# Kernel tuning notes

Hardware: AMD Instinct MI355X
Metric: run time of the kernel (lower is better)

Reference implementation:

```python
import jax, jax.numpy as jnp
import numpy as np

B, L, D_EMB, D_K, D_V, N_HEAD = 32, 512, 768, 512, 1024, 8
LN_EPS = 1e-6
MASK_FILL = 1e-9  # non-standard fill value from the original module


def setup_inputs() -> dict:
    key = jax.random.key(0)
    ks = jax.random.split(key, 13)
    s = 0.02
    return {
        "q": jax.random.normal(ks[0], (B, L, D_EMB), jnp.float32),
        "k": jax.random.normal(ks[1], (B, L, D_EMB), jnp.float32),
        "v": jax.random.normal(ks[2], (B, L, D_EMB), jnp.float32),
        "Wq": jax.random.normal(ks[3], (D_EMB, D_K), jnp.float32) * s,
        "Wk": jax.random.normal(ks[4], (D_EMB, D_K), jnp.float32) * s,
        "Wv": jax.random.normal(ks[5], (D_EMB, D_V), jnp.float32) * s,
        "Wconv": jax.random.normal(ks[6], (D_K, D_K), jnp.float32) * s,  # Conv1d k=1 (out_ch, in_ch)
        "bconv": jax.random.normal(ks[7], (D_K,), jnp.float32) * s,
        "Wfc": jax.random.normal(ks[8], (D_V, D_EMB), jnp.float32) * s,
        "gamma": jnp.ones((D_EMB,), jnp.float32),
        "beta": jnp.zeros((D_EMB,), jnp.float32),
        "mask1": jax.random.randint(ks[9], (B, L), 0, 2).astype(jnp.bool_),
        "mask2": jax.random.randint(ks[10], (B, L), 0, 2).astype(jnp.bool_),
    }


def reference(q, k, v, Wq, Wk, Wv, Wconv, bconv, Wfc, gamma, beta, mask1, mask2):
    Bq, Lq, _ = q.shape
    Lk = k.shape[1]
    dh_k = D_K // N_HEAD
    dh_v = D_V // N_HEAD
    residual = q

    # Q/K projections followed by the (buggy-but-faithful) Conv1d(k=1) that
    # treats the sequence axis as channels: out[b,o,l] = sum_c W[o,c]*x[b,c,l] + bias[o]
    q1 = q @ Wq                                   # (B, Lq, D_K)
    k1 = k @ Wk                                   # (B, Lk, D_K)
    q1 = jnp.einsum('oc,bcl->bol', Wconv, q1) + bconv[None, :, None]
    k1 = jnp.einsum('oc,bcl->bol', Wconv, k1) + bconv[None, :, None]
    v1 = v @ Wv                                   # (B, Lk, D_V)

    qh = q1.reshape(Bq, Lq, N_HEAD, dh_k).transpose(0, 2, 1, 3)  # (B,H,Lq,dk/H)
    kh = k1.reshape(Bq, Lk, N_HEAD, dh_k).transpose(0, 2, 1, 3)
    vh = v1.reshape(Bq, Lk, N_HEAD, dh_v).transpose(0, 2, 1, 3)

    temp = jnp.sqrt(jnp.asarray(D_K, qh.dtype))
    attn = jnp.einsum('bhqd,bhkd->bhqk', qh / temp, kh)          # (B,H,Lq,Lk)
    attn = jnp.where(mask1[:, None, :, None], MASK_FILL, attn)
    attn = jnp.where(mask2[:, None, None, :], MASK_FILL, attn)
    attn = jax.nn.softmax(attn, axis=-1)
    # dropout is identity in eval / deterministic reference

    out = jnp.einsum('bhqk,bhkd->bhqd', attn, vh)                # (B,H,Lq,dv/H)
    out = out.transpose(0, 2, 1, 3).reshape(Bq, Lq, D_V)
    out = out @ Wfc + residual                                   # (B,Lq,D_EMB)

    mu = out.mean(-1, keepdims=True)
    var = out.var(-1, keepdims=True)
    out = (out - mu) / jnp.sqrt(var + LN_EPS) * gamma + beta
    out = jnp.where(jnp.isnan(out), jnp.zeros((), out.dtype), out)
    return out, attn
```

## Files before the change

kernel.cpp:

```cpp
#include <hip/hip_runtime.h>

typedef short v8s __attribute__((ext_vector_type(8)));
typedef short v4s __attribute__((ext_vector_type(4)));
typedef float v4f __attribute__((ext_vector_type(4)));

#define BN 128
#define BK 64

__device__ __forceinline__ float b2f(unsigned short u) {
    union { unsigned int i; float f; } x; x.i = ((unsigned int)u) << 16; return x.f;
}
__device__ __forceinline__ unsigned short f2b(float f) {
    union { float f; unsigned int i; } x; x.f = f;
    unsigned int r = x.i + 0x7fffu + ((x.i >> 16) & 1u);
    return (unsigned short)(r >> 16);
}

__device__ __forceinline__ void gload16(const void* g, void* l) {
    __builtin_amdgcn_global_load_lds(
        (const __attribute__((address_space(1))) void*)g,
        (__attribute__((address_space(3))) void*)l, 16, 0, 0);
}

template<int EPI>
__device__ __forceinline__ void gemm_body(
    const unsigned short* __restrict__ A, int lda, long aOff,
    const unsigned short* __restrict__ BT, int ldb, long bOff,
    void* __restrict__ C, int ldc, long cOff, long cSBt,
    int K, const float* __restrict__ bias,
    const float* __restrict__ resid, int ldr,
    int bm, int bn)
{
    __shared__ unsigned short SM[49152];

    const int tid = threadIdx.x;
    const int wave = tid >> 6, lane = tid & 63;
    const int wm = (wave >> 1) * 64, wn = (wave & 1) * 64;
    const int quad = lane >> 4, l16 = lane & 15;
    const int sx = l16 & 7;

    const unsigned short* aP[4]; const unsigned short* bP[2];
    int aL[4], bL[2];
#pragma unroll
    for (int p = 0; p < 4; p++) {
        int idx = p * 512 + tid;
        int row = idx >> 3, c = idx & 7, cc = c ^ (row & 7);
        aP[p] = A + aOff + (long)(bm + row) * lda + cc * 8;
        aL[p] = idx * 8;
    }
#pragma unroll
    for (int p = 0; p < 2; p++) {
        int idx = p * 512 + tid;
        int row = idx >> 3, c = idx & 7, cc = c ^ (row & 7);
        bP[p] = BT + bOff + (long)(bn + row) * ldb + cc * 8;
        bL[p] = 16384 + idx * 8;
    }

    auto stage = [&](int t, int b) {
        const int k0 = t * BK;
        unsigned short* base = &SM[b * 24576];
#pragma unroll
        for (int p = 0; p < 4; p++) gload16(aP[p] + k0, base + aL[p]);
#pragma unroll
        for (int p = 0; p < 2; p++) gload16(bP[p] + k0, base + bL[p]);
    };

    v4f acc[4][4] = {};
    const int nt = K >> 6;

    stage(0, 0);
    stage(1, 1);

    for (int t = 0; t < nt; t++) {
        if (t + 1 < nt) asm volatile("s_waitcnt vmcnt(6)" ::: "memory");
        else            asm volatile("s_waitcnt vmcnt(0)" ::: "memory");
        __builtin_amdgcn_s_barrier();
        __builtin_amdgcn_sched_barrier(0);
        const unsigned short* As = &SM[(t & 1) * 24576];
        const unsigned short* Bs = As + 16384;
#pragma unroll
        for (int ks = 0; ks < 2; ks++) {
            v8s af[4], bf[4];
#pragma unroll
            for (int i = 0; i < 4; i++) {
                const int co = ((ks * 4 + quad) ^ sx) * 8;
                af[i] = *(const v8s*)&As[(wm + i * 16 + l16) * 64 + co];
                bf[i] = *(const v8s*)&Bs[(wn + i * 16 + l16) * 64 + co];
            }
#pragma unroll
            for (int i = 0; i < 4; i++)
#pragma unroll
                for (int j = 0; j < 4; j++)
                    acc[i][j] = __builtin_amdgcn_mfma_f32_16x16x32_bf16(af[i], bf[j], acc[i][j], 0, 0, 0);
        }
        __builtin_amdgcn_s_barrier();
        __builtin_amdgcn_sched_barrier(0);
        if (t + 2 < nt) stage(t + 2, t & 1);
    }

    if (EPI == 1) {
        const int bb = bm >> 9, mm0 = bm & 511;
        unsigned short* Cu = (unsigned short*)C + cOff + (long)bb * cSBt + mm0;
#pragma unroll
        for (int pass = 0; pass < 2; pass++) {
            __syncthreads();
            if ((wave & 1) == pass) {
#pragma unroll
                for (int i = 0; i < 4; i++) {
                    int mb = wm + i * 16 + quad * 4;
#pragma unroll
                    for (int j = 0; j < 4; j++) {
                        int n = j * 16 + l16;
                        unsigned int lo = (unsigned int)f2b(acc[i][j][0]) | ((unsigned int)f2b(acc[i][j][1]) << 16);
                        unsigned int hi = (unsigned int)f2b(acc[i][j][2]) | ((unsigned int)f2b(acc[i][j][3]) << 16);
                        *(unsigned int*)&SM[n * 264 + mb] = lo;
                        *(unsigned int*)&SM[n * 264 + mb + 2] = hi;
                    }
                }
            }
            __syncthreads();
            int row = tid >> 3, part = tid & 7;
            const uint4* s = (const uint4*)&SM[row * 264 + part * 32];
            uint4 v0 = s[0], v1 = s[1];
            uint4* d = (uint4*)&Cu[(long)(bn + pass * 64 + row) * ldc + part * 32];
            d[0] = v0; d[1] = v1;
        }
    } else {
        float* TF = (float*)SM;
        unsigned short* Cu = (unsigned short*)C + cOff;
#pragma unroll
        for (int pass = 0; pass < 4; pass++) {
            __syncthreads();
            if ((wave >> 1) == pass) {
#pragma unroll
                for (int i = 0; i < 4; i++) {
                    int rl = i * 16 + quad * 4;
#pragma unroll
                    for (int j = 0; j < 4; j++) {
                        int cl = wn + j * 16 + l16;
#pragma unroll
                        for (int r = 0; r < 4; r++)
                            TF[(rl + r) * 132 + cl] = acc[i][j][r];
                    }
                }
            }
            __syncthreads();
            int row = tid >> 3, part = tid & 7;
            int gm = bm + pass * 64 + row;
            const float* srcr = &TF[row * 132 + part * 16];
            float bs = (EPI == 2) ? bias[gm] : 0.f;
            const float* rr = (EPI == 4) ? &resid[(long)gm * ldr + bn + part * 16] : nullptr;
            unsigned short tmp[16];
#pragma unroll
            for (int e = 0; e < 16; e++) {
                float v = srcr[e];
                if (EPI == 2) v += bs;
                else v += rr[e];
                tmp[e] = f2b(v);
            }
            uint4* d = (uint4*)&Cu[(long)gm * ldc + bn + part * 16];
            d[0] = *(uint4*)&tmp[0];
            d[1] = *(uint4*)&tmp[8];
        }
    }
}

template<int EPI>
__global__ __launch_bounds__(512)
void gemm_bt(const unsigned short* __restrict__ A, int lda, long aSB,
             const unsigned short* __restrict__ BT, int ldb, long bSB,
             void* __restrict__ C, int ldc, long cSB,
             int K, const float* __restrict__ bias,
             const float* __restrict__ resid, int ldr)
{
    const int z = blockIdx.z;
    gemm_body<EPI>(A, lda, (long)z * aSB, BT, ldb, (long)z * bSB,
                   C, ldc, (long)z * cSB, cSB, K, bias, resid, ldr,
                   blockIdx.y * 256, blockIdx.x * BN);
}

__global__ __launch_bounds__(512)
void proj3_k(const unsigned short* __restrict__ qb, const unsigned short* __restrict__ kb,
             const unsigned short* __restrict__ vb,
             const unsigned short* __restrict__ WqT, const unsigned short* __restrict__ WkT,
             const unsigned short* __restrict__ WvT,
             unsigned short* __restrict__ q1t, unsigned short* __restrict__ k1t,
             unsigned short* __restrict__ v1t)
{
    const int x = blockIdx.x;
    const int bm = blockIdx.y * 256;
    if (x < 4) {
        gemm_body<1>(qb, 768, 0, WqT, 768, 0, q1t, 512, 0, 262144, 768,
                     nullptr, nullptr, 0, bm, x * BN);
    } else if (x < 8) {
        gemm_body<1>(kb, 768, 0, WkT, 768, 0, k1t, 512, 0, 262144, 768,
                     nullptr, nullptr, 0, bm, (x - 4) * BN);
    } else {
        gemm_body<1>(vb, 768, 0, WvT, 768, 0, v1t, 512, 0, 524288, 768,
                     nullptr, nullptr, 0, bm, (x - 8) * BN);
    }
}

__global__ __launch_bounds__(512)
void conv2_k(const unsigned short* __restrict__ Wconv_b,
             const unsigned short* __restrict__ q1t, const unsigned short* __restrict__ k1t,
             unsigned short* __restrict__ q1c, unsigned short* __restrict__ k1c,
             const float* __restrict__ bconv)
{
    const int z = blockIdx.z;
    const int b = z & 31, sel = z >> 5;
    const int bm = blockIdx.y * 256, bn = blockIdx.x * BN;
    const unsigned short* Bt = sel ? k1t : q1t;
    unsigned short* Cc = sel ? k1c : q1c;
    gemm_body<2>(Wconv_b, 512, 0, Bt, 512, (long)b * 262144,
                 Cc, 512, (long)b * 262144, 0, 512, bconv, nullptr, 0, bm, bn);
}

__global__ __launch_bounds__(512, 4)
void scores_pv_k(const unsigned short* __restrict__ q1c,
                 const unsigned short* __restrict__ k1c,
                 const unsigned short* __restrict__ v1t,
                 float* __restrict__ attn,
                 unsigned short* __restrict__ out1,
                 const int* __restrict__ mask1,
                 const int* __restrict__ mask2,
                 float scale)
{
    const int id = blockIdx.x;
    const int logical = (id & 7) * 128 + (id >> 3);
    const int z = logical >> 2;
    const int bx = logical & 3;
    const int b = z >> 3, h = z & 7;

    const unsigned short* Qb = q1c + (long)b * 262144 + h * 64;
    const unsigned short* Kb = k1c + (long)b * 262144 + h * 64;
    const unsigned short* Vb = v1t + (long)b * 524288 + (long)h * 65536;

    __shared__ unsigned short KA[128 * 64];
    __shared__ unsigned short VB[128 * 128];
    __shared__ unsigned short Pl[8][640];
    __shared__ int m2s[512];

    const int tid = threadIdx.x;
    const int wave = tid >> 6, lane = tid & 63;
    const int quad = lane >> 4, l16 = lane & 15;
    const int sx = l16 & 7;
    const int bm = bx * 128;
    const int row_l = wave * 16 + l16;
    const int qrow = bm + row_l;

    auto stageK = [&](int kt, unsigned short* dst) {
#pragma unroll
        for (int p = 0; p < 2; p++) {
            int idx = p * 512 + tid;
            int row = idx >> 3, c = idx & 7, cc = c ^ (row & 7);
            gload16(Kb + (long)(kt * 128 + row) * 512 + cc * 8, &dst[idx * 8]);
        }
    };
    auto stageV = [&](int kt) {
#pragma unroll
        for (int p = 0; p < 4; p++) {
            int idx = p * 512 + tid;
            int dv = idx >> 4, c = idx & 15, cc = c ^ (dv & 7);
            gload16(Vb + (long)dv * 512 + kt * 128 + cc * 8, &VB[idx * 8]);
        }
    };

    stageK(0, KA);
    m2s[tid] = mask2[b * 512 + tid];

    v8s qf0 = *(const v8s*)&Qb[(long)qrow * 512 + quad * 8];
    v8s qf1 = *(const v8s*)&Qb[(long)qrow * 512 + 32 + quad * 8];
    const int m1 = mask1[b * 512 + qrow];

    __syncthreads();

    float sum = 0.f;

    for (int kt = 0; kt < 4; kt++) {
        const unsigned short* cur = (kt & 1) ? &VB[0] : KA;
        if (kt < 3) stageK(kt + 1, (kt & 1) ? KA : &VB[0]);
        else        stageK(0, KA);
#pragma unroll
        for (int jl = 0; jl < 8; jl++) {
            const unsigned short* kr = &cur[(jl * 16 + l16) * 64];
            v8s kf0 = *(const v8s*)&kr[(quad ^ sx) << 3];
            v8s kf1 = *(const v8s*)&kr[((4 + quad) ^ sx) << 3];
            v4f a = (v4f){0.f, 0.f, 0.f, 0.f};
            a = __builtin_amdgcn_mfma_f32_16x16x32_bf16(kf0, qf0, a, 0, 0, 0);
            a = __builtin_amdgcn_mfma_f32_16x16x32_bf16(kf1, qf1, a, 0, 0, 0);
            int j = kt * 8 + jl;
            int4 m2v = *(const int4*)&m2s[j * 16 + quad * 4];
            float s0 = (m1 != 0 || m2v.x != 0) ? 1e-9f : a[0] * scale;
            float s1 = (m1 != 0 || m2v.y != 0) ? 1e-9f : a[1] * scale;
            float s2 = (m1 != 0 || m2v.z != 0) ? 1e-9f : a[2] * scale;
            float s3 = (m1 != 0 || m2v.w != 0) ? 1e-9f : a[3] * scale;
            sum += (__expf(s0) + __expf(s1)) + (__expf(s2) + __expf(s3));
        }
        __syncthreads();
    }
    sum += __shfl_xor(sum, 16, 64);
    sum += __shfl_xor(sum, 32, 64);
    const float inv = 1.0f / sum;

    float* Arow = attn + (long)z * 262144 + (long)qrow * 512;
    unsigned short* Pw = &Pl[wave][l16 * 40];
    v4f acc2[8];
#pragma unroll
    for (int t = 0; t < 8; t++) acc2[t] = (v4f){0.f, 0.f, 0.f, 0.f};

    for (int kt = 0; kt < 4; kt++) {
        if (kt > 0) stageK(kt, KA);
        stageV(kt);
        __syncthreads();

#pragma unroll
        for (int g = 0; g < 4; g++) {
            float p8[8];
#pragma unroll
            for (int t2 = 0; t2 < 2; t2++) {
                int jl = g * 2 + t2;
                const unsigned short* kr = &KA[(jl * 16 + l16) * 64];
                v8s kf0 = *(const v8s*)&kr[(quad ^ sx) << 3];
                v8s kf1 = *(const v8s*)&kr[((4 + quad) ^ sx) << 3];
                v4f a = (v4f){0.f, 0.f, 0.f, 0.f};
                a = __builtin_amdgcn_mfma_f32_16x16x32_bf16(kf0, qf0, a, 0, 0, 0);
                a = __builtin_amdgcn_mfma_f32_16x16x32_bf16(kf1, qf1, a, 0, 0, 0);
                int j = kt * 8 + jl;
                int4 m2v = *(const int4*)&m2s[j * 16 + quad * 4];
                float s0 = (m1 != 0 || m2v.x != 0) ? 1e-9f : a[0] * scale;
                float s1 = (m1 != 0 || m2v.y != 0) ? 1e-9f : a[1] * scale;
                float s2 = (m1 != 0 || m2v.z != 0) ? 1e-9f : a[2] * scale;
                float s3 = (m1 != 0 || m2v.w != 0) ? 1e-9f : a[3] * scale;
                p8[t2 * 4 + 0] = __expf(s0) * inv;
                p8[t2 * 4 + 1] = __expf(s1) * inv;
                p8[t2 * 4 + 2] = __expf(s2) * inv;
                p8[t2 * 4 + 3] = __expf(s3) * inv;
            }
            int j0 = kt * 8 + g * 2;
            uint2 pr0, pr1;
            pr0.x = (unsigned int)f2b(p8[0]) | ((unsigned int)f2b(p8[1]) << 16);
            pr0.y = (unsigned int)f2b(p8[2]) | ((unsigned int)f2b(p8[3]) << 16);
            pr1.x = (unsigned int)f2b(p8[4]) | ((unsigned int)f2b(p8[5]) << 16);
            pr1.y = (unsigned int)f2b(p8[6]) | ((unsigned int)f2b(p8[7]) << 16);
            *(uint2*)&Pw[quad * 4] = pr0;
            *(uint2*)&Pw[16 + quad * 4] = pr1;
            v4f w0; w0[0] = p8[0]; w0[1] = p8[1]; w0[2] = p8[2]; w0[3] = p8[3];
            v4f w1; w1[0] = p8[4]; w1[1] = p8[5]; w1[2] = p8[6]; w1[3] = p8[7];
            __builtin_nontemporal_store(w0, (v4f*)&Arow[j0 * 16 + quad * 4]);
            __builtin_nontemporal_store(w1, (v4f*)&Arow[(j0 + 1) * 16 + quad * 4]);
            v8s pf = *(const v8s*)&Pw[quad * 8];
#pragma unroll
            for (int t = 0; t < 8; t++) {
                v8s vf = *(const v8s*)&VB[(t * 16 + l16) * 128 + (((g * 4 + quad) ^ sx) << 3)];
                acc2[t] = __builtin_amdgcn_mfma_f32_16x16x32_bf16(vf, pf, acc2[t], 0, 0, 0);
            }
        }
        __syncthreads();
    }

    unsigned short* Orow = out1 + (long)b * 524288 + (long)qrow * 1024 + h * 128;
#pragma unroll
    for (int t = 0; t < 8; t++) {
        v4s o;
        o[0] = (short)f2b(acc2[t][0]); o[1] = (short)f2b(acc2[t][1]);
        o[2] = (short)f2b(acc2[t][2]); o[3] = (short)f2b(acc2[t][3]);
        *(v4s*)&Orow[t * 16 + quad * 4] = o;
    }
}

__global__ __launch_bounds__(256)
void prep_k(const float* __restrict__ Wq, const float* __restrict__ Wk,
            const float* __restrict__ Wv, const float* __restrict__ Wfc,
            const float* __restrict__ Wconv,
            const float* __restrict__ qf, const float* __restrict__ kf,
            const float* __restrict__ vf,
            unsigned short* __restrict__ WqT, unsigned short* __restrict__ WkT,
            unsigned short* __restrict__ WvT, unsigned short* __restrict__ WfcT,
            unsigned short* __restrict__ Wconv_b,
            unsigned short* __restrict__ qb, unsigned short* __restrict__ kb,
            unsigned short* __restrict__ vb)
{
    __shared__ float t[32][33];
    int blk = blockIdx.x, tid = threadIdx.x;
    if (blk < 2304) {
        const float* src; unsigned short* dst; int K, N, local;
        if (blk < 384)       { src = Wq;  dst = WqT;  K = 768;  N = 512;  local = blk; }
        else if (blk < 768)  { src = Wk;  dst = WkT;  K = 768;  N = 512;  local = blk - 384; }
        else if (blk < 1536) { src = Wv;  dst = WvT;  K = 768;  N = 1024; local = blk - 768; }
        else                 { src = Wfc; dst = WfcT; K = 1024; N = 768;  local = blk - 1536; }
        int nb32 = N >> 5;
        int kb32 = (local / nb32) * 32, nb = (local % nb32) * 32;
        int tx = tid & 31, ty = tid >> 5;
#pragma unroll
        for (int i = 0; i < 32; i += 8)
            t[ty + i][tx] = src[(long)(kb32 + ty + i) * N + nb + tx];
        __syncthreads();
#pragma unroll
        for (int i = 0; i < 32; i += 8)
            dst[(long)(nb + ty + i) * K + kb32 + tx] = f2b(t[tx][ty + i]);
    } else if (blk < 3328) {
        int i = (blk - 2304) * 256 + tid;
        Wconv_b[i] = f2b(Wconv[i]);
    } else {
        long t0 = (long)(blk - 3328) * 4096 + (long)tid * 16;
        const float* src; unsigned short* dst; long i = t0;
        if (t0 < 12582912L)       { src = qf; dst = qb; }
        else if (t0 < 25165824L)  { src = kf; dst = kb; i = t0 - 12582912L; }
        else                      { src = vf; dst = vb; i = t0 - 25165824L; }
        v4f a = __builtin_nontemporal_load((const v4f*)&src[i]);
        v4f b4 = __builtin_nontemporal_load((const v4f*)&src[i + 4]);
        v4f c4 = __builtin_nontemporal_load((const v4f*)&src[i + 8]);
        v4f d4 = __builtin_nontemporal_load((const v4f*)&src[i + 12]);
        v8s r0, r1;
        r0[0] = (short)f2b(a[0]);  r0[1] = (short)f2b(a[1]);
        r0[2] = (short)f2b(a[2]);  r0[3] = (short)f2b(a[3]);
        r0[4] = (short)f2b(b4[0]); r0[5] = (short)f2b(b4[1]);
        r0[6] = (short)f2b(b4[2]); r0[7] = (short)f2b(b4[3]);
        r1[0] = (short)f2b(c4[0]); r1[1] = (short)f2b(c4[1]);
        r1[2] = (short)f2b(c4[2]); r1[3] = (short)f2b(c4[3]);
        r1[4] = (short)f2b(d4[0]); r1[5] = (short)f2b(d4[1]);
        r1[6] = (short)f2b(d4[2]); r1[7] = (short)f2b(d4[3]);
        *(v8s*)&dst[i] = r0;
        *(v8s*)&dst[i + 8] = r1;
    }
}

__global__ __launch_bounds__(256)
void ln_k(const unsigned short* __restrict__ x,
          const float* __restrict__ gamma,
          const float* __restrict__ beta,
          float* __restrict__ out)
{
    long row = (long)blockIdx.x * 4 + (threadIdx.x >> 6);
    int lane = threadIdx.x & 63;
    const unsigned short* p = x + row * 768;
    v8s a = *(const v8s*)&p[lane * 8];
    v4s b4 = *(const v4s*)&p[512 + lane * 4];
    float v[12];
    float s = 0.f, s2 = 0.f;
#pragma unroll
    for (int j = 0; j < 8; j++) { v[j] = b2f((unsigned short)a[j]); s += v[j]; s2 += v[j] * v[j]; }
#pragma unroll
    for (int j = 0; j < 4; j++) { v[8 + j] = b2f((unsigned short)b4[j]); s += v[8 + j]; s2 += v[8 + j] * v[8 + j]; }
#pragma unroll
    for (int o = 32; o > 0; o >>= 1) { s += __shfl_xor(s, o, 64); s2 += __shfl_xor(s2, o, 64); }
    float mean = s * (1.0f / 768.0f);
    float var = s2 * (1.0f / 768.0f) - mean * mean;
    if (!(var >= 0.f)) var = 0.f;
    float rstd = rsqrtf(var + 1e-6f);
    float o12[12];
#pragma unroll
    for (int j = 0; j < 8; j++) {
        int c = lane * 8 + j;
        float o = (v[j] - mean) * rstd * gamma[c] + beta[c];
        union { float f; unsigned int i; } uu; uu.f = o;
        if ((uu.i & 0x7FFFFFFFu) > 0x7F800000u) uu.f = 0.f;
        o12[j] = uu.f;
    }
#pragma unroll
    for (int j = 0; j < 4; j++) {
        int c = 512 + lane * 4 + j;
        float o = (v[8 + j] - mean) * rstd * gamma[c] + beta[c];
        union { float f; unsigned int i; } uu; uu.f = o;
        if ((uu.i & 0x7FFFFFFFu) > 0x7F800000u) uu.f = 0.f;
        o12[8 + j] = uu.f;
    }
    v4f f0; f0[0] = o12[0]; f0[1] = o12[1]; f0[2] = o12[2]; f0[3] = o12[3];
    v4f f1; f1[0] = o12[4]; f1[1] = o12[5]; f1[2] = o12[6]; f1[3] = o12[7];
    v4f f2; f2[0] = o12[8]; f2[1] = o12[9]; f2[2] = o12[10]; f2[3] = o12[11];
    __builtin_nontemporal_store(f0, (v4f*)&out[row * 768 + lane * 8]);
    __builtin_nontemporal_store(f1, (v4f*)&out[row * 768 + lane * 8 + 4]);
    __builtin_nontemporal_store(f2, (v4f*)&out[row * 768 + 512 + lane * 4]);
}

extern "C" void kernel_launch(void* const* d_in, const int* in_sizes, int n_in,
                              void* d_out, int out_size, void* d_ws, size_t ws_size,
                              hipStream_t stream)
{
    const float* q     = (const float*)d_in[0];
    const float* k     = (const float*)d_in[1];
    const float* v     = (const float*)d_in[2];
    const float* Wq    = (const float*)d_in[3];
    const float* Wk    = (const float*)d_in[4];
    const float* Wv    = (const float*)d_in[5];
    const float* Wconv = (const float*)d_in[6];
    const float* bconv = (const float*)d_in[7];
    const float* Wfc   = (const float*)d_in[8];
    const float* gamma = (const float*)d_in[9];
    const float* beta  = (const float*)d_in[10];
    const int* mask1   = (const int*)d_in[11];
    const int* mask2   = (const int*)d_in[12];

    float* out  = (float*)d_out;
    float* attn = out + 12582912;

    unsigned short* ws = (unsigned short*)d_ws;
    unsigned short* WqT     = ws;
    unsigned short* WkT     = ws + 393216;
    unsigned short* WvT     = ws + 786432;
    unsigned short* WfcT    = ws + 1572864;
    unsigned short* Wconv_b = ws + 2359296;
    unsigned short* q1c     = ws + 2621440;
    unsigned short* k1c     = ws + 11010048;
    unsigned short* v1t     = ws + 19398656;
    unsigned short* out2    = ws + 19398656;

    unsigned short* aScr = (unsigned short*)attn;
    unsigned short* q1t = aScr;
    unsigned short* k1t = aScr + 8388608;
    unsigned short* qb  = aScr + 16777216;
    unsigned short* kb  = aScr + 29360128;
    unsigned short* vb  = aScr + 41943040;
    unsigned short* out1 = (unsigned short*)out;

    prep_k<<<12544, 256, 0, stream>>>(Wq, Wk, Wv, Wfc, Wconv, q, k, v,
                                      WqT, WkT, WvT, WfcT, Wconv_b, qb, kb, vb);

    const float scale = 0.04419417382415922f;

    proj3_k<<<dim3(16, 64, 1), 512, 0, stream>>>(
        qb, kb, vb, WqT, WkT, WvT, q1t, k1t, v1t);

    conv2_k<<<dim3(4, 2, 64), 512, 0, stream>>>(
        Wconv_b, q1t, k1t, q1c, k1c, bconv);

    scores_pv_k<<<1024, 512, 0, stream>>>(
        q1c, k1c, v1t, attn, out1, mask1, mask2, scale);

    gemm_bt<4><<<dim3(6, 64, 1), 512, 0, stream>>>(
        out1, 1024, 0, WfcT, 1024, 0, out2, 768, 0, 1024, nullptr, q, 768);

    ln_k<<<4096, 256, 0, stream>>>(out2, gamma, beta, out);
}
```

Measured before the change: 659.9 us.

## Fuse FC projection, residual add and LayerNorm into one kernel

Replaces the separate Wfc GEMM (bf16 output) and LayerNorm kernel with one kernel. Each block computes a full 64x768 row tile and does the residual add and row statistics across waves through shared memory, then writes the normalized fp32 output directly. This removes the bf16 round-trip of the intermediate and one launch. The trade is a much smaller grid (256 blocks), a single-buffered K loop with no prefetch, and heavy LDS use, which may lower GEMM throughput. It also moves the out1 buffer into the workspace because the output can no longer serve as scratch.

```diff
diff --git a/kernel.cpp b/kernel.cpp
--- a/kernel.cpp
+++ b/kernel.cpp
@@ -163,20 +163,6 @@
             d[1] = *(uint4*)&tmp[8];
         }
     }
-}
-
-template<int EPI>
-__global__ __launch_bounds__(512)
-void gemm_bt(const unsigned short* __restrict__ A, int lda, long aSB,
-             const unsigned short* __restrict__ BT, int ldb, long bSB,
-             void* __restrict__ C, int ldc, long cSB,
-             int K, const float* __restrict__ bias,
-             const float* __restrict__ resid, int ldr)
-{
-    const int z = blockIdx.z;
-    gemm_body<EPI>(A, lda, (long)z * aSB, BT, ldb, (long)z * bSB,
-                   C, ldc, (long)z * cSB, cSB, K, bias, resid, ldr,
-                   blockIdx.y * 256, blockIdx.x * BN);
 }
 
 __global__ __launch_bounds__(512)
@@ -214,6 +200,137 @@
     unsigned short* Cc = sel ? k1c : q1c;
     gemm_body<2>(Wconv_b, 512, 0, Bt, 512, (long)b * 262144,
                  Cc, 512, (long)b * 262144, 0, 512, bconv, nullptr, 0, bm, bn);
+}
+
+__global__ __launch_bounds__(512)
+void fc_ln_k(const unsigned short* __restrict__ out1,
+             const unsigned short* __restrict__ WfcT,
+             const float* __restrict__ resid,
+             const float* __restrict__ gamma,
+             const float* __restrict__ beta,
+             float* __restrict__ out)
+{
+    __shared__ unsigned short SM[53248];
+
+    const int tid = threadIdx.x;
+    const int wave = tid >> 6, lane = tid & 63;
+    const int quad = lane >> 4, l16 = lane & 15;
+    const int sx = l16 & 7;
+    const int bm = blockIdx.x * 64;
+    const int wn = wave * 96;
+
+    const int arow = tid >> 3, ac = tid & 7;
+    const unsigned short* aP = out1 + (long)(bm + arow) * 1024 + (ac ^ (arow & 7)) * 8;
+    const int aL = tid * 8;
+
+    v4f acc[4][6] = {};
+
+    for (int k0 = 0; k0 < 1024; k0 += 64) {
+        gload16(aP + k0, &SM[aL]);
+#pragma unroll
+        for (int p = 0; p < 12; p++) {
+            int idx = p * 512 + tid;
+            int row = idx >> 3, c = idx & 7, cc = c ^ (row & 7);
+            gload16(WfcT + (long)row * 1024 + cc * 8 + k0, &SM[4096 + idx * 8]);
+        }
+        __syncthreads();
+#pragma unroll
+        for (int ks = 0; ks < 2; ks++) {
+            const int co = ((ks * 4 + quad) ^ sx) * 8;
+            v8s af[4], bf[6];
+#pragma unroll
+            for (int i = 0; i < 4; i++)
+                af[i] = *(const v8s*)&SM[(i * 16 + l16) * 64 + co];
+#pragma unroll
+            for (int j = 0; j < 6; j++)
+                bf[j] = *(const v8s*)&SM[4096 + (wn + j * 16 + l16) * 64 + co];
+#pragma unroll
+            for (int i = 0; i < 4; i++)
+#pragma unroll
+                for (int j = 0; j < 6; j++)
+                    acc[i][j] = __builtin_amdgcn_mfma_f32_16x16x32_bf16(af[i], bf[j], acc[i][j], 0, 0, 0);
+        }
+        __syncthreads();
+    }
+
+    float g6[6], be6[6];
+#pragma unroll
+    for (int j = 0; j < 6; j++) {
+        g6[j] = gamma[wn + j * 16 + l16];
+        be6[j] = beta[wn + j * 16 + l16];
+    }
+
+    float rs[4][4] = {{0.f}}, rq[4][4] = {{0.f}};
+#pragma unroll
+    for (int i = 0; i < 4; i++)
+#pragma unroll
+        for (int r = 0; r < 4; r++) {
+            int gm = bm + i * 16 + quad * 4 + r;
+            const float* rr = &resid[(long)gm * 768 + wn + l16];
+#pragma unroll
+            for (int j = 0; j < 6; j++) {
+                float v = acc[i][j][r] + rr[j * 16];
+                acc[i][j][r] = v;
+                rs[i][r] += v;
+                rq[i][r] += v * v;
+            }
+        }
+#pragma unroll
+    for (int off = 1; off < 16; off <<= 1)
+#pragma unroll
+        for (int i = 0; i < 4; i++)
+#pragma unroll
+            for (int r = 0; r < 4; r++) {
+                rs[i][r] += __shfl_xor(rs[i][r], off, 64);
+                rq[i][r] += __shfl_xor(rq[i][r], off, 64);
+            }
+
+    float* ST = (float*)SM;
+    if (l16 == 0) {
+#pragma unroll
+        for (int i = 0; i < 4; i++)
+#pragma unroll
+            for (int r = 0; r < 4; r++) {
+                int row = i * 16 + quad * 4 + r;
+                ST[row * 8 + wave] = rs[i][r];
+                ST[512 + row * 8 + wave] = rq[i][r];
+            }
+    }
+    __syncthreads();
+
+    float mean[4][4], rstd[4][4];
+#pragma unroll
+    for (int i = 0; i < 4; i++)
+#pragma unroll
+        for (int r = 0; r < 4; r++) {
+            int row = i * 16 + quad * 4 + r;
+            float s = 0.f, s2 = 0.f;
+#pragma unroll
+            for (int w = 0; w < 8; w++) {
+                s += ST[row * 8 + w];
+                s2 += ST[512 + row * 8 + w];
+            }
+            float m = s * (1.0f / 768.0f);
+            float var = s2 * (1.0f / 768.0f) - m * m;
+            if (!(var >= 0.f)) var = 0.f;
+            mean[i][r] = m;
+            rstd[i][r] = rsqrtf(var + 1e-6f);
+        }
+
+#pragma unroll
+    for (int i = 0; i < 4; i++)
+#pragma unroll
+        for (int r = 0; r < 4; r++) {
+            int gm = bm + i * 16 + quad * 4 + r;
+            float* orow = &out[(long)gm * 768 + wn + l16];
+#pragma unroll
+            for (int j = 0; j < 6; j++) {
+                float o = (acc[i][j][r] - mean[i][r]) * rstd[i][r] * g6[j] + be6[j];
+                union { float f; unsigned int u; } uu; uu.f = o;
+                if ((uu.u & 0x7FFFFFFFu) > 0x7F800000u) uu.f = 0.f;
+                orow[j * 16] = uu.f;
+            }
+        }
 }
 
 __global__ __launch_bounds__(512, 4)
@@ -426,54 +543,6 @@
     }
 }
 
-__global__ __launch_bounds__(256)
-void ln_k(const unsigned short* __restrict__ x,
-          const float* __restrict__ gamma,
-          const float* __restrict__ beta,
-          float* __restrict__ out)
-{
-    long row = (long)blockIdx.x * 4 + (threadIdx.x >> 6);
-    int lane = threadIdx.x & 63;
-    const unsigned short* p = x + row * 768;
-    v8s a = *(const v8s*)&p[lane * 8];
-    v4s b4 = *(const v4s*)&p[512 + lane * 4];
-    float v[12];
-    float s = 0.f, s2 = 0.f;
-#pragma unroll
-    for (int j = 0; j < 8; j++) { v[j] = b2f((unsigned short)a[j]); s += v[j]; s2 += v[j] * v[j]; }
-#pragma unroll
-    for (int j = 0; j < 4; j++) { v[8 + j] = b2f((unsigned short)b4[j]); s += v[8 + j]; s2 += v[8 + j] * v[8 + j]; }
-#pragma unroll
-    for (int o = 32; o > 0; o >>= 1) { s += __shfl_xor(s, o, 64); s2 += __shfl_xor(s2, o, 64); }
-    float mean = s * (1.0f / 768.0f);
-    float var = s2 * (1.0f / 768.0f) - mean * mean;
-    if (!(var >= 0.f)) var = 0.f;
-    float rstd = rsqrtf(var + 1e-6f);
-    float o12[12];
-#pragma unroll
-    for (int j = 0; j < 8; j++) {
-        int c = lane * 8 + j;
-        float o = (v[j] - mean) * rstd * gamma[c] + beta[c];
-        union { float f; unsigned int i; } uu; uu.f = o;
-        if ((uu.i & 0x7FFFFFFFu) > 0x7F800000u) uu.f = 0.f;
-        o12[j] = uu.f;
-    }
-#pragma unroll
-    for (int j = 0; j < 4; j++) {
-        int c = 512 + lane * 4 + j;
-        float o = (v[8 + j] - mean) * rstd * gamma[c] + beta[c];
-        union { float f; unsigned int i; } uu; uu.f = o;
-        if ((uu.i & 0x7FFFFFFFu) > 0x7F800000u) uu.f = 0.f;
-        o12[8 + j] = uu.f;
-    }
-    v4f f0; f0[0] = o12[0]; f0[1] = o12[1]; f0[2] = o12[2]; f0[3] = o12[3];
-    v4f f1; f1[0] = o12[4]; f1[1] = o12[5]; f1[2] = o12[6]; f1[3] = o12[7];
-    v4f f2; f2[0] = o12[8]; f2[1] = o12[9]; f2[2] = o12[10]; f2[3] = o12[11];
-    __builtin_nontemporal_store(f0, (v4f*)&out[row * 768 + lane * 8]);
-    __builtin_nontemporal_store(f1, (v4f*)&out[row * 768 + lane * 8 + 4]);
-    __builtin_nontemporal_store(f2, (v4f*)&out[row * 768 + 512 + lane * 4]);
-}
-
 extern "C" void kernel_launch(void* const* d_in, const int* in_sizes, int n_in,
                               void* d_out, int out_size, void* d_ws, size_t ws_size,
                               hipStream_t stream)
@@ -504,7 +573,7 @@
     unsigned short* q1c     = ws + 2621440;
     unsigned short* k1c     = ws + 11010048;
     unsigned short* v1t     = ws + 19398656;
-    unsigned short* out2    = ws + 19398656;
+    unsigned short* out1    = ws + 36175872;
 
     unsigned short* aScr = (unsigned short*)attn;
     unsigned short* q1t = aScr;
@@ -512,7 +581,6 @@
     unsigned short* qb  = aScr + 16777216;
     unsigned short* kb  = aScr + 29360128;
     unsigned short* vb  = aScr + 41943040;
-    unsigned short* out1 = (unsigned short*)out;
 
     prep_k<<<12544, 256, 0, stream>>>(Wq, Wk, Wv, Wfc, Wconv, q, k, v,
                                       WqT, WkT, WvT, WfcT, Wconv_b, qb, kb, vb);
@@ -528,8 +596,5 @@
     scores_pv_k<<<1024, 512, 0, stream>>>(
         q1c, k1c, v1t, attn, out1, mask1, mask2, scale);
 
-    gemm_bt<4><<<dim3(6, 64, 1), 512, 0, stream>>>(
-        out1, 1024, 0, WfcT, 1024, 0, out2, 768, 0, 1024, nullptr, q, 768);
-
-    ln_k<<<4096, 256, 0, stream>>>(out2, gamma, beta, out);
-}
+    fc_ln_k<<<256, 512, 0, stream>>>(out1, WfcT, q, gamma, beta, out);
+}
```

Result: no change. 647.6 us (-1.9%).
